# Kernel optimization log

Measured on AMD Instinct MI355X. Metric: run time of the kernel, lower is better.

Reference implementation:

```python
import jax, jax.numpy as jnp
import numpy as np
from jax import lax

BOS, EOS = 62, 63
NEG_BIG = -10000.0


def setup_inputs() -> dict:
    key = jax.random.key(0)
    k_em, k_tag, k_len, k_tr = jax.random.split(key, 4)
    B, S, L = 512, 1024, 64
    emissions = jax.random.normal(k_em, (B, S, L), dtype=jnp.float32)
    tags = jax.random.randint(k_tag, (B, S), 0, 62).astype(jnp.int64)
    # valid-prefix mask from random lengths in [S//2, S]
    lengths = jax.random.randint(k_len, (B,), S // 2, S + 1)
    mask = (jnp.arange(S)[None, :] < lengths[:, None]).astype(jnp.float32)
    # transitions: uniform(-0.1, 0.1) with BOS/EOS constraints as in init_weights
    transitions = jax.random.uniform(k_tr, (L, L), minval=-0.1, maxval=0.1, dtype=jnp.float32)
    transitions = transitions.at[:, BOS].set(NEG_BIG)
    transitions = transitions.at[EOS, :].set(NEG_BIG)
    return {"emissions": emissions, "tags": tags, "mask": mask, "transitions": transitions}


def _crf_nll(emissions, tags, mask, transitions):
    B, S, L = emissions.shape
    # ----- gold-path scores -----
    first_tags = tags[:, 0]
    last_idx = (mask.sum(axis=1).astype(jnp.int32) - 1)  # (B,)
    last_tags = jnp.take_along_axis(tags, last_idx[:, None].astype(tags.dtype), axis=1)[:, 0]
    scores = transitions[BOS, first_tags]
    scores = scores + jnp.take_along_axis(emissions[:, 0], first_tags[:, None], axis=1)[:, 0]
    prev_t, cur_t = tags[:, :-1], tags[:, 1:]
    e_step = jnp.take_along_axis(emissions[:, 1:], cur_t[..., None], axis=-1)[..., 0]  # (B,S-1)
    t_step = transitions[prev_t, cur_t]  # (B,S-1)
    scores = scores + jnp.sum((e_step + t_step) * mask[:, 1:], axis=1)
    scores = scores + transitions[last_tags, EOS]
    # ----- log-partition via forward algorithm -----
    alpha0 = transitions[BOS][None, :] + emissions[:, 0]  # (B,L)
    em_t = jnp.moveaxis(emissions[:, 1:], 1, 0)  # (S-1,B,L)
    mk_t = mask[:, 1:].T  # (S-1,B)

    def step(alpha, xs):
        e_t, m_t = xs
        # alpha[b,i] + T[i,j] + e_t[b,j] -> logsumexp over i
        new = jax.nn.logsumexp(alpha[:, :, None] + transitions[None, :, :] + e_t[:, None, :], axis=1)
        return jnp.where(m_t[:, None] > 0, new, alpha), None

    alpha, _ = lax.scan(step, alpha0, (em_t, mk_t))
    partition = jax.nn.logsumexp(alpha + transitions[:, EOS][None, :], axis=1)  # (B,)
    return -jnp.sum(scores - partition)


def reference(emissions, tags, mask, transitions):
    return _crf_nll(emissions, tags, mask, transitions)
```

## Files before the change

kernel.cpp:

```cpp
#include <hip/hip_runtime.h>
#include <math.h>

#define BOS_TAG 62
#define EOS_TAG 63
#define S_LEN   1024
#define NCH     64
#define CH      16
#define WPB     4
#define LN2F    0.69314718055994530942f

typedef short  short8 __attribute__((ext_vector_type(8)));
typedef unsigned short ushort4v __attribute__((ext_vector_type(4)));
typedef float  f32x4  __attribute__((ext_vector_type(4)));

template <int CTRL>
__device__ __forceinline__ int dpp_mov(int v) {
  return __builtin_amdgcn_update_dpp(v, v, CTRL, 0xf, 0xf, false);
}
template <int CTRL>
__device__ __forceinline__ float dpp_fmax_step(float v) {
  return fmaxf(v, __int_as_float(dpp_mov<CTRL>(__float_as_int(v))));
}
__device__ __forceinline__ float wave_fmax_all(float v) {
  v = dpp_fmax_step<0x111>(v); v = dpp_fmax_step<0x112>(v);
  v = dpp_fmax_step<0x114>(v); v = dpp_fmax_step<0x118>(v);
  v = dpp_fmax_step<0x142>(v); v = dpp_fmax_step<0x143>(v);
  return __int_as_float(__builtin_amdgcn_readlane(__float_as_int(v), 63));
}
template <int CTRL>
__device__ __forceinline__ float dpp_fadd_step(float v) {
  int t = __builtin_amdgcn_update_dpp(0, __float_as_int(v), CTRL, 0xf, 0xf, true);
  return v + __int_as_float(t);
}
__device__ __forceinline__ float wave_sum_all(float v) {
  v = dpp_fadd_step<0x111>(v); v = dpp_fadd_step<0x112>(v);
  v = dpp_fadd_step<0x114>(v); v = dpp_fadd_step<0x118>(v);
  v = dpp_fadd_step<0x142>(v); v = dpp_fadd_step<0x143>(v);
  return __int_as_float(__builtin_amdgcn_readlane(__float_as_int(v), 63));
}
__device__ __forceinline__ unsigned short f2bf(float v) {
  return (unsigned short)((__float_as_uint(v) + 0x8000u) >> 16);
}
__device__ __forceinline__ float bf2f(unsigned short u) {
  return __uint_as_float(((unsigned)u) << 16);
}

__global__ __launch_bounds__(256) void crf_lens(
    const float* __restrict__ mask, int* __restrict__ lens, int B)
{
  const int b = blockIdx.x * 4 + (threadIdx.x >> 6);
  if (b >= B) return;
  const int l = threadIdx.x & 63;
  const float4* mb = (const float4*)(mask + (size_t)b * S_LEN);
  float s = 0.f;
#pragma unroll
  for (int i = 0; i < 4; ++i) { float4 q = mb[l + 64 * i]; s += q.x + q.y + q.z + q.w; }
  s = wave_sum_all(s);
  if (l == 0) lens[b] = max(1, min(S_LEN, (int)(s + 0.5f)));
}

__global__ __launch_bounds__(256) void crf_ptab(
    const float* __restrict__ trans, short8* __restrict__ pfrag,
    float* __restrict__ tvf)
{
  const int tid = threadIdx.x;
  for (int e = tid; e < 1024; e += 256) {
    int lane = e & 63, n = (e >> 6) & 3, kc = (e >> 8) & 1, dir = e >> 9;
    int g = lane >> 4, c = lane & 15, col = 4 * c + n;
    short8 f;
#pragma unroll
    for (int j = 0; j < 8; ++j) {
      int k = kc * 32 + g * 8 + j;
      float tv = dir ? trans[col * 64 + k] : trans[k * 64 + col];
      f[j] = (short)f2bf(__expf(tv));
    }
    pfrag[e] = f;
  }
  if (tid < 64) tvf[tid] = __expf(trans[tid * 64 + EOS_TAG]);
}

__global__ __launch_bounds__(256, 3) void crf_chunk_mfma(
    const float* __restrict__ em, const float* __restrict__ trans,
    const int* __restrict__ lens, const short8* __restrict__ pfrag,
    unsigned short* __restrict__ Vf, unsigned short* __restrict__ Vb,
    float* __restrict__ sf, float* __restrict__ sb,
    float* __restrict__ m0a, int B)
{
  __shared__ unsigned short smem[4][16 * 64];
  const int wv = threadIdx.x >> 6;
  const int l  = threadIdx.x & 63;
  const int w  = blockIdx.x * 4 + wv;
  const int nwaves = 2 * B * WPB;
  if (w >= nwaves) return;
  const int dir  = w & 1;
  const int idx  = w >> 1;
  const int b    = idx / WPB;
  const int half = idx % WPB;
  unsigned short* smw = smem[wv];
  const float* embase = em + (size_t)b * S_LEN * 64;
  const int g = l >> 4, c = l & 15;

  const int len = lens[b];

  float v_row0 = 1.0f;
  if (dir == 0 && half == 0) {
    float a0 = trans[BOS_TAG * 64 + l] + embase[l];
    float m0 = wave_fmax_all(a0);
    v_row0 = __expf(a0 - m0);
    if (l == 0) m0a[b] = m0;
  }

  unsigned short* Vout = dir ? Vb : Vf;
  float* sout = dir ? sb : sf;
  int fstep[16];
  int ps = -1, pr = -1;
#pragma unroll
  for (int r = 0; r < 16; ++r) {
    int kg = half * 16 + r;
    int tend = min((kg + 1) * CH, len - 1);
    fstep[r] = tend - (kg * CH + 1);
    if (fstep[r] < 0) {
      Vout[((size_t)b * NCH + kg) * 64 + l] = 0x3F80;
      if (l == 0) sout[b * NCH + kg] = 0.f;
    }
    if (fstep[r] >= 0 && fstep[r] < CH - 1) { ps = fstep[r]; pr = r; }
  }

  if (half * 16 * CH + 1 > len - 1) return;

  short8 Bf[2][4];
  {
    const short8* pf = pfrag + dir * 512;
#pragma unroll
    for (int kc = 0; kc < 2; ++kc)
#pragma unroll
      for (int n = 0; n < 4; ++n)
        Bf[kc][n] = pf[(kc * 4 + n) * 64 + l];
  }

#pragma unroll
  for (int r = 0; r < 16; ++r) {
    float v = (dir == 0 && half == 0 && r == 0) ? v_row0 : 1.0f;
    smw[(r * 64 + l) ^ ((r & 7) << 3)] = f2bf(v);
  }

  const int byteA0 = (c * 128 + g * 16) ^ ((c & 7) << 4);
  const int byteA1 = (c * 128 + 64 + g * 16) ^ ((c & 7) << 4);
  int sigma = 0;

  auto renorm16 = [&](float* d) {
    float m = d[0];
#pragma unroll
    for (int i = 1; i < 16; ++i) m = fmaxf(m, d[i]);
    m = wave_fmax_all(m);
    int e = ((__float_as_int(m) >> 23) & 0xff) - 127;
    float s = __int_as_float((127 - e) << 23);
#pragma unroll
    for (int i = 0; i < 16; ++i) d[i] *= s;
    sigma += e;
  };
  auto save_row = [&](int r) {
    unsigned short v = smw[(r * 64 + l) ^ ((r & 7) << 3)];
    int kg = half * 16 + r;
    Vout[((size_t)b * NCH + kg) * 64 + l] = v;
    if (l == 0) sout[b * NCH + kg] = (float)sigma;
  };
  auto write_d = [&](const float* d) {
#pragma unroll
    for (int reg = 0; reg < 4; ++reg) {
      int row = g * 4 + reg;
      ushort4v wq;
#pragma unroll
      for (int n = 0; n < 4; ++n) wq[n] = f2bf(d[reg * 4 + n]);
      *reinterpret_cast<ushort4v*>(
          (char*)smw + ((row * 128 + c * 8) ^ ((row & 7) << 4))) = wq;
    }
  };

  if (dir == 0) {
    int tb0[4];
#pragma unroll
    for (int reg = 0; reg < 4; ++reg) tb0[reg] = (half * 16 + g * 4 + reg) * CH + 1;

    auto loadF = [&](float4* q, int tl) {
#pragma unroll
      for (int reg = 0; reg < 4; ++reg) {
        int tr = min(tb0[reg] + tl, S_LEN - 1);
        q[reg] = *reinterpret_cast<const float4*>(embase + (size_t)tr * 64 + 4 * c);
      }
    };
    auto bodyF = [&](const float4* q, int tl, bool rn) {
      short8 a0 = *reinterpret_cast<const short8*>((const char*)smw + byteA0);
      short8 a1 = *reinterpret_cast<const short8*>((const char*)smw + byteA1);
      f32x4 acc[4];
#pragma unroll
      for (int n = 0; n < 4; ++n) {
        f32x4 z = {0.f, 0.f, 0.f, 0.f};
        z = __builtin_amdgcn_mfma_f32_16x16x32_bf16(a0, Bf[0][n], z, 0, 0, 0);
        acc[n] = __builtin_amdgcn_mfma_f32_16x16x32_bf16(a1, Bf[1][n], z, 0, 0, 0);
      }
      float d[16];
#pragma unroll
      for (int reg = 0; reg < 4; ++reg) {
        d[reg * 4 + 0] = acc[0][reg] * __expf(q[reg].x);
        d[reg * 4 + 1] = acc[1][reg] * __expf(q[reg].y);
        d[reg * 4 + 2] = acc[2][reg] * __expf(q[reg].z);
        d[reg * 4 + 3] = acc[3][reg] * __expf(q[reg].w);
      }
      if (rn) renorm16(d);
      write_d(d);
      if (tl == ps) save_row(pr);
    };

    float4 p0[4], p1[4], p2[4], p3[4];
    loadF(p0, 0); loadF(p1, 1); loadF(p2, 2); loadF(p3, 3);
#pragma unroll 1
    for (int t4 = 0; t4 < CH; t4 += 4) {
      bodyF(p0, t4 + 0, false); loadF(p0, t4 + 4);
      bodyF(p1, t4 + 1, false); loadF(p1, t4 + 5);
      bodyF(p2, t4 + 2, false); loadF(p2, t4 + 6);
      bodyF(p3, t4 + 3, true);  loadF(p3, t4 + 7);
    }
#pragma unroll
    for (int r = 0; r < 16; ++r)
      if (fstep[r] == CH - 1) save_row(r);
  } else {
    const int tendl = min((half * 16 + c + 1) * CH, len - 1);

    auto loadB = [&](float4* q, int tl) {
      int tr = max(tendl - tl, 0);
      const float* rowp = embase + (size_t)tr * 64;
      q[0] = *reinterpret_cast<const float4*>(rowp + 8 * g);
      q[1] = *reinterpret_cast<const float4*>(rowp + 8 * g + 4);
      q[2] = *reinterpret_cast<const float4*>(rowp + 32 + 8 * g);
      q[3] = *reinterpret_cast<const float4*>(rowp + 32 + 8 * g + 4);
    };
    auto bodyB = [&](const float4* q, int tl, bool rn) {
      short8 ar0 = *reinterpret_cast<const short8*>((const char*)smw + byteA0);
      short8 ar1 = *reinterpret_cast<const short8*>((const char*)smw + byteA1);
      short8 a0, a1;
#pragma unroll
      for (int j = 0; j < 4; ++j) {
        a0[j]     = (short)f2bf(bf2f((unsigned short)ar0[j])     * __expf(((const float*)&q[0])[j]));
        a0[4 + j] = (short)f2bf(bf2f((unsigned short)ar0[4 + j]) * __expf(((const float*)&q[1])[j]));
        a1[j]     = (short)f2bf(bf2f((unsigned short)ar1[j])     * __expf(((const float*)&q[2])[j]));
        a1[4 + j] = (short)f2bf(bf2f((unsigned short)ar1[4 + j]) * __expf(((const float*)&q[3])[j]));
      }
      f32x4 acc[4];
#pragma unroll
      for (int n = 0; n < 4; ++n) {
        f32x4 z = {0.f, 0.f, 0.f, 0.f};
        z = __builtin_amdgcn_mfma_f32_16x16x32_bf16(a0, Bf[0][n], z, 0, 0, 0);
        acc[n] = __builtin_amdgcn_mfma_f32_16x16x32_bf16(a1, Bf[1][n], z, 0, 0, 0);
      }
      float d[16];
#pragma unroll
      for (int reg = 0; reg < 4; ++reg)
#pragma unroll
        for (int n = 0; n < 4; ++n) d[reg * 4 + n] = acc[n][reg];
      if (rn) renorm16(d);
      write_d(d);
      if (tl == ps) save_row(pr);
    };

    float4 p0[4], p1[4], p2[4], p3[4];
    loadB(p0, 0); loadB(p1, 1); loadB(p2, 2); loadB(p3, 3);
#pragma unroll 1
    for (int t4 = 0; t4 < CH; t4 += 4) {
      bodyB(p0, t4 + 0, false); loadB(p0, t4 + 4);
      bodyB(p1, t4 + 1, false); loadB(p1, t4 + 5);
      bodyB(p2, t4 + 2, false); loadB(p2, t4 + 6);
      bodyB(p3, t4 + 3, true);  loadB(p3, t4 + 7);
    }
#pragma unroll
    for (int r = 0; r < 16; ++r)
      if (fstep[r] == CH - 1) save_row(r);
  }
}

__global__ __launch_bounds__(256) void crf_combine(
    const float* __restrict__ em, const int* __restrict__ tags,
    const float* __restrict__ trans, const int* __restrict__ lens,
    const unsigned short* __restrict__ Vf, const unsigned short* __restrict__ Vb,
    const float* __restrict__ sf, const float* __restrict__ sb,
    const float* __restrict__ m0a, const float* __restrict__ tvf,
    float* __restrict__ term, int B)
{
  const int item = blockIdx.x * 4 + (threadIdx.x >> 6);
  if (item >= B * NCH) return;
  const int b = item / NCH, k = item - b * NCH;
  const int l = threadIdx.x & 63;
  const int len = lens[b];
  const int kb = (len >= 2) ? (len - 2) / CH : 0;

  const int* tb = tags + (size_t)b * S_LEN;
  const float* emb = em + (size_t)b * S_LEN * 64;

  float t = 0.f;
  {
    float sc = 0.f;
    int t0 = k * CH + 1 + l;
    if (l < CH && t0 <= len - 1) {
      int cur = tb[t0], prev = tb[t0 - 1];
      sc = emb[(size_t)t0 * 64 + cur] + trans[prev * 64 + cur];
    }
    if (k == 0) {
      if (l == 32) sc += trans[BOS_TAG * 64 + tb[0]] + emb[tb[0]];
      if (l == 33) sc += trans[tb[len - 1] * 64 + EOS_TAG];
    }
    t -= wave_sum_all(sc);
  }

  const unsigned short* vf = Vf + ((size_t)b * NCH + k) * 64;
  if (k == 0) {
    float v0 = bf2f(vf[l]);
    if (kb == 0) {
      t += m0a[b] + LN2F * sf[b * NCH] + __logf(wave_sum_all(v0 * tvf[l]));
    } else {
      t += m0a[b] + LN2F * (sf[b * NCH] + sb[b * NCH + 1])
         + __logf(wave_sum_all(v0 * bf2f(Vb[((size_t)b * NCH + 1) * 64 + l])));
    }
  } else if (k < kb) {
    float vk = bf2f(vf[l]);
    t += LN2F * sb[b * NCH + k + 1]
       + __logf(wave_sum_all(vk * bf2f(Vb[((size_t)b * NCH + k + 1) * 64 + l])))
       - __logf(wave_sum_all(vk));
  } else if (k == kb) {
    float vk = bf2f(vf[l]);
    t += __logf(wave_sum_all(vk * tvf[l])) - __logf(wave_sum_all(vk));
  }

  if (l == 0) term[item] = t;
}

__global__ __launch_bounds__(1024) void crf_final(
    const float* __restrict__ term, float* __restrict__ out, int n)
{
  __shared__ float red[16];
  float s = 0.f;
  for (int i = threadIdx.x; i < n; i += 1024) s += term[i];
  s = wave_sum_all(s);
  const int wid = threadIdx.x >> 6;
  if ((threadIdx.x & 63) == 0) red[wid] = s;
  __syncthreads();
  if (threadIdx.x == 0) {
    float tot = 0.f;
#pragma unroll
    for (int i = 0; i < 16; ++i) tot += red[i];
    out[0] = tot;
  }
}

__global__ __launch_bounds__(64) void crf_mono(
    const float* __restrict__ em, const int* __restrict__ tags,
    const float* __restrict__ mask, const float* __restrict__ trans,
    float* __restrict__ partial)
{
  const int b = blockIdx.x;
  const int l = threadIdx.x;
  const float* emb = em + (size_t)b * S_LEN * 64;
  const float* mb = mask + (size_t)b * S_LEN;
  float lenf = 0.f;
  for (int t = l; t < S_LEN; t += 64) lenf += mb[t];
  lenf = wave_sum_all(lenf);
  const int len = max(1, min(S_LEN, (int)(lenf + 0.5f)));

  float p[64];
#pragma unroll
  for (int i = 0; i < 64; ++i) p[i] = __expf(trans[i * 64 + l]) * 0.015625f;

  const int* tb = tags + (size_t)b * S_LEN;
  float sc = 0.f;
  for (int tt = 1 + l; tt <= len - 1; tt += 64)
    sc += emb[(size_t)tt * 64 + tb[tt]] + trans[tb[tt - 1] * 64 + tb[tt]];
  sc = wave_sum_all(sc);
  sc += trans[BOS_TAG * 64 + tb[0]] + emb[tb[0]] + trans[tb[len - 1] * 64 + EOS_TAG];

  float a0 = trans[BOS_TAG * 64 + l] + emb[l];
  float m0 = wave_fmax_all(a0);
  float v = __expf(a0 - m0);
  int sigma = 0;
  for (int t = 1; t <= len - 1; ++t) {
    float E = __expf(emb[(size_t)t * 64 + l]);
    int xi = __float_as_int(v);
    float s0 = 0.f, s1 = 0.f, s2 = 0.f, s3 = 0.f;
#pragma unroll
    for (int i = 0; i < 64; i += 4) {
      s0 = fmaf(__int_as_float(__builtin_amdgcn_readlane(xi, i + 0)), p[i + 0], s0);
      s1 = fmaf(__int_as_float(__builtin_amdgcn_readlane(xi, i + 1)), p[i + 1], s1);
      s2 = fmaf(__int_as_float(__builtin_amdgcn_readlane(xi, i + 2)), p[i + 2], s2);
      s3 = fmaf(__int_as_float(__builtin_amdgcn_readlane(xi, i + 3)), p[i + 3], s3);
    }
    v = ((s0 + s1) + (s2 + s3)) * E;
    float m = wave_fmax_all(v);
    int e = ((__float_as_int(m) >> 23) & 0xff) - 127;
    sigma += e + 6;
    v *= __int_as_float((127 - e) << 23);
  }
  float tvec = __expf(trans[l * 64 + EOS_TAG]);
  float lp = m0 + LN2F * (float)sigma + __logf(wave_sum_all(v * tvec));
  if (l == 0) partial[b] = lp - sc;
}

extern "C" void kernel_launch(void* const* d_in, const int* in_sizes, int n_in,
                              void* d_out, int out_size, void* d_ws, size_t ws_size,
                              hipStream_t stream) {
  const float* em = (const float*)d_in[0];
  const int* tags = (const int*)d_in[1];
  const float* mask = (const float*)d_in[2];
  const float* trans = (const float*)d_in[3];
  float* out = (float*)d_out;

  const int B = in_sizes[1] / S_LEN;

  const size_t nSig = (size_t)B * NCH;
  const size_t nV   = (size_t)B * NCH * 64;
  const size_t need = 16384 + 64 * sizeof(float)
                    + (3 * nSig + (size_t)B) * sizeof(float)
                    + (size_t)B * sizeof(int)
                    + 2 * nV * sizeof(unsigned short);

  if (ws_size >= need) {
    short8* pfrag = (short8*)d_ws;
    float* tvf  = (float*)((char*)d_ws + 16384);
    float* sf   = tvf + 64;
    float* sb   = sf + nSig;
    float* m0a  = sb + nSig;
    float* term = m0a + B;
    int*   lens = (int*)(term + nSig);
    unsigned short* Vf = (unsigned short*)(lens + B);
    unsigned short* Vb = Vf + nV;

    crf_lens<<<(B + 3) / 4, 256, 0, stream>>>(mask, lens, B);
    crf_ptab<<<1, 256, 0, stream>>>(trans, pfrag, tvf);
    const int nwaves = 2 * B * WPB;
    crf_chunk_mfma<<<(nwaves + 3) / 4, 256, 0, stream>>>(
        em, trans, lens, pfrag, Vf, Vb, sf, sb, m0a, B);
    crf_combine<<<(B * NCH + 3) / 4, 256, 0, stream>>>(
        em, tags, trans, lens, Vf, Vb, sf, sb, m0a, tvf, term, B);
    crf_final<<<1, 1024, 0, stream>>>(term, out, B * NCH);
  } else {
    float* partial = (float*)d_ws;
    crf_mono<<<B, 64, 0, stream>>>(em, tags, mask, trans, partial);
    crf_final<<<1, 1024, 0, stream>>>(partial, out, B);
  }
}
```

Baseline: 76.63 us.

## Restructure backward chunk recurrence to scale MFMA output, use packed bf16 converts

The backward direction is reformulated so the emission scaling is applied to the MFMA accumulator output, as in the forward pass, instead of unpacking, scaling and repacking the A operand before each MFMA. The first emission row is folded into the initial LDS state and the final step becomes an epilogue MFMA that writes directly to global memory. Float-to-bf16 packing now uses the v_cvt_pk_bf16_f32 instruction, and launch bounds are raised to 4 blocks per CU. The aim is to cut VALU conversion work on the serial critical path and raise occupancy. The risks are register spills from the tighter launch bound and small changes in bf16 rounding.

```diff
diff --git a/kernel.cpp b/kernel.cpp
--- a/kernel.cpp
+++ b/kernel.cpp
@@ -10,7 +10,6 @@
 #define LN2F    0.69314718055994530942f
 
 typedef short  short8 __attribute__((ext_vector_type(8)));
-typedef unsigned short ushort4v __attribute__((ext_vector_type(4)));
 typedef float  f32x4  __attribute__((ext_vector_type(4)));
 
 template <int CTRL>
@@ -44,6 +43,11 @@
 __device__ __forceinline__ float bf2f(unsigned short u) {
   return __uint_as_float(((unsigned)u) << 16);
 }
+__device__ __forceinline__ unsigned pk2(float lo, float hi) {
+  unsigned r;
+  asm("v_cvt_pk_bf16_f32 %0, %1, %2" : "=v"(r) : "v"(lo), "v"(hi));
+  return r;
+}
 
 __global__ __launch_bounds__(256) void crf_lens(
     const float* __restrict__ mask, int* __restrict__ lens, int B)
@@ -79,7 +83,7 @@
   if (tid < 64) tvf[tid] = __expf(trans[tid * 64 + EOS_TAG]);
 }
 
-__global__ __launch_bounds__(256, 3) void crf_chunk_mfma(
+__global__ __launch_bounds__(256, 4) void crf_chunk_mfma(
     const float* __restrict__ em, const float* __restrict__ trans,
     const int* __restrict__ lens, const short8* __restrict__ pfrag,
     unsigned short* __restrict__ Vf, unsigned short* __restrict__ Vb,
@@ -138,12 +142,6 @@
         Bf[kc][n] = pf[(kc * 4 + n) * 64 + l];
   }
 
-#pragma unroll
-  for (int r = 0; r < 16; ++r) {
-    float v = (dir == 0 && half == 0 && r == 0) ? v_row0 : 1.0f;
-    smw[(r * 64 + l) ^ ((r & 7) << 3)] = f2bf(v);
-  }
-
   const int byteA0 = (c * 128 + g * 16) ^ ((c & 7) << 4);
   const int byteA1 = (c * 128 + 64 + g * 16) ^ ((c & 7) << 4);
   int sigma = 0;
@@ -159,46 +157,52 @@
     for (int i = 0; i < 16; ++i) d[i] *= s;
     sigma += e;
   };
-  auto save_row = [&](int r) {
+  auto mfma8 = [&](f32x4* acc) {
+    short8 a0 = *reinterpret_cast<const short8*>((const char*)smw + byteA0);
+    short8 a1 = *reinterpret_cast<const short8*>((const char*)smw + byteA1);
+#pragma unroll
+    for (int n = 0; n < 4; ++n) {
+      f32x4 z = {0.f, 0.f, 0.f, 0.f};
+      z = __builtin_amdgcn_mfma_f32_16x16x32_bf16(a0, Bf[0][n], z, 0, 0, 0);
+      acc[n] = __builtin_amdgcn_mfma_f32_16x16x32_bf16(a1, Bf[1][n], z, 0, 0, 0);
+    }
+  };
+  auto write_d = [&](const float* d) {
+#pragma unroll
+    for (int reg = 0; reg < 4; ++reg) {
+      int row = g * 4 + reg;
+      uint2 wq;
+      wq.x = pk2(d[reg * 4 + 0], d[reg * 4 + 1]);
+      wq.y = pk2(d[reg * 4 + 2], d[reg * 4 + 3]);
+      *reinterpret_cast<uint2*>(
+          (char*)smw + ((row * 128 + c * 8) ^ ((row & 7) << 4))) = wq;
+    }
+  };
+  auto save_row_lds = [&](int r) {
     unsigned short v = smw[(r * 64 + l) ^ ((r & 7) << 3)];
     int kg = half * 16 + r;
     Vout[((size_t)b * NCH + kg) * 64 + l] = v;
     if (l == 0) sout[b * NCH + kg] = (float)sigma;
   };
-  auto write_d = [&](const float* d) {
+
+  int tb0[4];
+#pragma unroll
+  for (int reg = 0; reg < 4; ++reg) {
+    int kg = half * 16 + g * 4 + reg;
+    tb0[reg] = dir ? (min((kg + 1) * CH, len - 1) - 1) : (kg * CH + 1);
+  }
+  auto loadE = [&](float4* q, int tl) {
 #pragma unroll
     for (int reg = 0; reg < 4; ++reg) {
-      int row = g * 4 + reg;
-      ushort4v wq;
-#pragma unroll
-      for (int n = 0; n < 4; ++n) wq[n] = f2bf(d[reg * 4 + n]);
-      *reinterpret_cast<ushort4v*>(
-          (char*)smw + ((row * 128 + c * 8) ^ ((row & 7) << 4))) = wq;
+      int tr = dir ? max(tb0[reg] - tl, 0) : min(tb0[reg] + tl, S_LEN - 1);
+      q[reg] = *reinterpret_cast<const float4*>(embase + (size_t)tr * 64 + 4 * c);
     }
   };
 
   if (dir == 0) {
-    int tb0[4];
-#pragma unroll
-    for (int reg = 0; reg < 4; ++reg) tb0[reg] = (half * 16 + g * 4 + reg) * CH + 1;
-
-    auto loadF = [&](float4* q, int tl) {
-#pragma unroll
-      for (int reg = 0; reg < 4; ++reg) {
-        int tr = min(tb0[reg] + tl, S_LEN - 1);
-        q[reg] = *reinterpret_cast<const float4*>(embase + (size_t)tr * 64 + 4 * c);
-      }
-    };
     auto bodyF = [&](const float4* q, int tl, bool rn) {
-      short8 a0 = *reinterpret_cast<const short8*>((const char*)smw + byteA0);
-      short8 a1 = *reinterpret_cast<const short8*>((const char*)smw + byteA1);
       f32x4 acc[4];
-#pragma unroll
-      for (int n = 0; n < 4; ++n) {
-        f32x4 z = {0.f, 0.f, 0.f, 0.f};
-        z = __builtin_amdgcn_mfma_f32_16x16x32_bf16(a0, Bf[0][n], z, 0, 0, 0);
-        acc[n] = __builtin_amdgcn_mfma_f32_16x16x32_bf16(a1, Bf[1][n], z, 0, 0, 0);
-      }
+      mfma8(acc);
       float d[16];
 #pragma unroll
       for (int reg = 0; reg < 4; ++reg) {
@@ -209,72 +213,86 @@
       }
       if (rn) renorm16(d);
       write_d(d);
-      if (tl == ps) save_row(pr);
+      if (tl == ps) save_row_lds(pr);
     };
 
+#pragma unroll
+    for (int r = 0; r < 16; ++r) {
+      float v = (half == 0 && r == 0) ? v_row0 : 1.0f;
+      smw[(r * 64 + l) ^ ((r & 7) << 3)] = f2bf(v);
+    }
+
     float4 p0[4], p1[4], p2[4], p3[4];
-    loadF(p0, 0); loadF(p1, 1); loadF(p2, 2); loadF(p3, 3);
+    loadE(p0, 0); loadE(p1, 1); loadE(p2, 2); loadE(p3, 3);
 #pragma unroll 1
     for (int t4 = 0; t4 < CH; t4 += 4) {
-      bodyF(p0, t4 + 0, false); loadF(p0, t4 + 4);
-      bodyF(p1, t4 + 1, false); loadF(p1, t4 + 5);
-      bodyF(p2, t4 + 2, false); loadF(p2, t4 + 6);
-      bodyF(p3, t4 + 3, true);  loadF(p3, t4 + 7);
+      bodyF(p0, t4 + 0, false); loadE(p0, t4 + 4);
+      bodyF(p1, t4 + 1, false); loadE(p1, t4 + 5);
+      bodyF(p2, t4 + 2, false); loadE(p2, t4 + 6);
+      bodyF(p3, t4 + 3, true);  loadE(p3, t4 + 7);
     }
 #pragma unroll
     for (int r = 0; r < 16; ++r)
-      if (fstep[r] == CH - 1) save_row(r);
+      if (fstep[r] == CH - 1) save_row_lds(r);
   } else {
-    const int tendl = min((half * 16 + c + 1) * CH, len - 1);
-
-    auto loadB = [&](float4* q, int tl) {
-      int tr = max(tendl - tl, 0);
-      const float* rowp = embase + (size_t)tr * 64;
-      q[0] = *reinterpret_cast<const float4*>(rowp + 8 * g);
-      q[1] = *reinterpret_cast<const float4*>(rowp + 8 * g + 4);
-      q[2] = *reinterpret_cast<const float4*>(rowp + 32 + 8 * g);
-      q[3] = *reinterpret_cast<const float4*>(rowp + 32 + 8 * g + 4);
+    auto epi_save = [&](bool finalAll) {
+      f32x4 acc[4];
+      mfma8(acc);
+#pragma unroll
+      for (int reg = 0; reg < 4; ++reg) {
+        int r = 4 * g + reg;
+        bool doit = finalAll ? (fstep[r] == CH - 1) : (r == pr);
+        if (doit) {
+          uint2 val;
+          val.x = pk2(acc[0][reg], acc[1][reg]);
+          val.y = pk2(acc[2][reg], acc[3][reg]);
+          *reinterpret_cast<uint2*>(
+              Vout + ((size_t)b * NCH + half * 16 + r) * 64 + 4 * c) = val;
+        }
+      }
+      if (finalAll) {
+        if (l < 16 && fstep[l] == CH - 1)
+          sout[b * NCH + half * 16 + l] = (float)sigma;
+      } else if (l == 0) {
+        sout[b * NCH + half * 16 + pr] = (float)sigma;
+      }
     };
     auto bodyB = [&](const float4* q, int tl, bool rn) {
-      short8 ar0 = *reinterpret_cast<const short8*>((const char*)smw + byteA0);
-      short8 ar1 = *reinterpret_cast<const short8*>((const char*)smw + byteA1);
-      short8 a0, a1;
-#pragma unroll
-      for (int j = 0; j < 4; ++j) {
-        a0[j]     = (short)f2bf(bf2f((unsigned short)ar0[j])     * __expf(((const float*)&q[0])[j]));
-        a0[4 + j] = (short)f2bf(bf2f((unsigned short)ar0[4 + j]) * __expf(((const float*)&q[1])[j]));
-        a1[j]     = (short)f2bf(bf2f((unsigned short)ar1[j])     * __expf(((const float*)&q[2])[j]));
-        a1[4 + j] = (short)f2bf(bf2f((unsigned short)ar1[4 + j]) * __expf(((const float*)&q[3])[j]));
+      f32x4 acc[4];
+      mfma8(acc);
+      float d[16];
+#pragma unroll
+      for (int reg = 0; reg < 4; ++reg) {
+        d[reg * 4 + 0] = acc[0][reg] * __expf(q[reg].x);
+        d[reg * 4 + 1] = acc[1][reg] * __expf(q[reg].y);
+        d[reg * 4 + 2] = acc[2][reg] * __expf(q[reg].z);
+        d[reg * 4 + 3] = acc[3][reg] * __expf(q[reg].w);
       }
-      f32x4 acc[4];
-#pragma unroll
-      for (int n = 0; n < 4; ++n) {
-        f32x4 z = {0.f, 0.f, 0.f, 0.f};
-        z = __builtin_amdgcn_mfma_f32_16x16x32_bf16(a0, Bf[0][n], z, 0, 0, 0);
-        acc[n] = __builtin_amdgcn_mfma_f32_16x16x32_bf16(a1, Bf[1][n], z, 0, 0, 0);
-      }
-      float d[16];
-#pragma unroll
-      for (int reg = 0; reg < 4; ++reg)
-#pragma unroll
-        for (int n = 0; n < 4; ++n) d[reg * 4 + n] = acc[n][reg];
       if (rn) renorm16(d);
       write_d(d);
-      if (tl == ps) save_row(pr);
+      if (tl == ps - 1) epi_save(false);
     };
 
+#pragma unroll
+    for (int r = 0; r < 16; ++r) {
+      int kg = half * 16 + r;
+      int tendr = min((kg + 1) * CH, len - 1);
+      float v = (fstep[r] >= 0) ? __expf(embase[(size_t)tendr * 64 + l]) : 1.0f;
+      smw[(r * 64 + l) ^ ((r & 7) << 3)] = f2bf(v);
+    }
+    if (ps == 0) epi_save(false);
+
     float4 p0[4], p1[4], p2[4], p3[4];
-    loadB(p0, 0); loadB(p1, 1); loadB(p2, 2); loadB(p3, 3);
+    loadE(p0, 0); loadE(p1, 1); loadE(p2, 2); loadE(p3, 3);
 #pragma unroll 1
-    for (int t4 = 0; t4 < CH; t4 += 4) {
-      bodyB(p0, t4 + 0, false); loadB(p0, t4 + 4);
-      bodyB(p1, t4 + 1, false); loadB(p1, t4 + 5);
-      bodyB(p2, t4 + 2, false); loadB(p2, t4 + 6);
-      bodyB(p3, t4 + 3, true);  loadB(p3, t4 + 7);
-    }
-#pragma unroll
-    for (int r = 0; r < 16; ++r)
-      if (fstep[r] == CH - 1) save_row(r);
+    for (int t4 = 0; t4 < 12; t4 += 4) {
+      bodyB(p0, t4 + 0, false); loadE(p0, t4 + 4);
+      bodyB(p1, t4 + 1, false); loadE(p1, t4 + 5);
+      bodyB(p2, t4 + 2, false); loadE(p2, t4 + 6);
+      bodyB(p3, t4 + 3, true);  loadE(p3, t4 + 7);
+    }
+    bodyB(p0, 12, false); bodyB(p1, 13, false); bodyB(p2, 14, false);
+    epi_save(true);
   }
 }
 
```

After: 172.5 us. 125% more time.
